# Performance work log

Measured on AMD Instinct MI355X. Metric: run time of the kernel, lower is better.

## Reference

```python
import jax, jax.numpy as jnp
import numpy as np

N = 100_000   # total vertices
E = 1_600_000 # total directed edges
B = 64        # graphs in batch
HID = 128
DM = 256
EPS = 1e-5


def _linear_init(k, fan_in, fan_out):
    lim = 1.0 / np.sqrt(fan_in)
    kw, kb = jax.random.split(k)
    W = jax.random.uniform(kw, (fan_in, fan_out), minval=-lim, maxval=lim, dtype=jnp.float32)
    b = jax.random.uniform(kb, (fan_out,), minval=-lim, maxval=lim, dtype=jnp.float32)
    return W, b


def setup_inputs() -> dict:
    key = jax.random.key(0)
    ks = jax.random.split(key, 8)
    W_in, b_in = _linear_init(ks[0], 3, HID)
    W1, b1 = _linear_init(ks[1], HID, HID)
    W2, b2 = _linear_init(ks[2], HID, HID)
    W3, b3 = _linear_init(ks[3], HID, HID)
    W_out, b_out = _linear_init(ks[4], HID, DM)
    vertices = jax.random.normal(ks[5], (N, 3), dtype=jnp.float32)
    edge_index = jax.random.randint(ks[6], (2, E), 0, N)
    batch = jnp.sort(jax.random.randint(ks[7], (N,), 0, B))
    gamma = jnp.ones((DM,), jnp.float32)
    beta = jnp.zeros((DM,), jnp.float32)
    return dict(vertices=vertices, edge_index=edge_index, batch=batch,
                W_in=W_in, b_in=b_in, W1=W1, b1=b1, W2=W2, b2=b2, W3=W3, b3=b3,
                W_out=W_out, b_out=b_out, gamma=gamma, beta=beta)


def _gcn_conv(x, W, b, src, dst):
    # PyG GCNConv: add self-loops, sym-normalize by deg^{-1/2}, aggregate at dst.
    h = x @ W  # [N, HID]
    deg = jnp.zeros((x.shape[0],), x.dtype).at[dst].add(1.0) + 1.0  # +1 self-loop
    dinv = jax.lax.rsqrt(deg)
    msg = h[src] * (dinv[src] * dinv[dst])[:, None]       # [E, HID] gather+scale
    agg = jnp.zeros_like(h).at[dst].add(msg)               # scatter-add
    agg = agg + h * (dinv * dinv)[:, None]                 # self-loop contribution
    return agg + b


def reference(vertices, edge_index, batch, W_in, b_in, W1, b1, W2, b2, W3, b3, W_out, b_out, gamma, beta):
    src, dst = edge_index[0], edge_index[1]
    x = vertices @ W_in + b_in
    for W, b in ((W1, b1), (W2, b2), (W3, b3)):
        x = jax.nn.relu(_gcn_conv(x, W, b, src, dst))
    # global_mean_pool over batch segments
    summ = jax.ops.segment_sum(x, batch, num_segments=B)
    cnt = jax.ops.segment_sum(jnp.ones((x.shape[0], 1), x.dtype), batch, num_segments=B)
    pooled = summ / jnp.maximum(cnt, 1.0)
    y = pooled @ W_out + b_out
    mu = jnp.mean(y, axis=-1, keepdims=True)
    var = jnp.var(y, axis=-1, keepdims=True)
    return (y - mu) * jax.lax.rsqrt(var + EPS) * gamma + beta
```

## Files before the change

kernel.cpp:

```cpp
#include <hip/hip_runtime.h>

constexpr int NV = 100000;
constexpr int NE = 1600000;
constexpr int NB = 64;
constexpr int HD = 128;
constexpr int DM = 256;
#define EPSLN 1e-5f

constexpr int DPB   = 512;
constexpr int NBUCK = (NV + DPB - 1) / DPB;
constexpr int EPB   = 4096;
constexpr int NEB   = (NE + EPB - 1) / EPB;

typedef short bf16x8 __attribute__((ext_vector_type(8)));
typedef float f32x4 __attribute__((ext_vector_type(4)));

__device__ inline unsigned short f2b(float f) {
    union { float f; unsigned u; } x; x.f = f;
    unsigned r = x.u + 0x7FFF + ((x.u >> 16) & 1);
    return (unsigned short)(r >> 16);
}
__device__ inline float b2f(unsigned short h) {
    union { unsigned u; float f; } x; x.u = (unsigned)h << 16;
    return x.f;
}

__global__ __launch_bounds__(256) void k_bhist(const int* __restrict__ ei,
                                               int* __restrict__ bcount) {
    __shared__ int h[NBUCK];
    int t = threadIdx.x;
    for (int i = t; i < NBUCK; i += 256) h[i] = 0;
    __syncthreads();
    int base = blockIdx.x * EPB;
    #pragma unroll
    for (int j = 0; j < EPB / 256; ++j) {
        int idx = base + j * 256 + t;
        if (idx < NE) atomicAdd(&h[ei[NE + idx] >> 9], 1);
    }
    __syncthreads();
    for (int i = t; i < NBUCK; i += 256) if (h[i]) atomicAdd(&bcount[i], h[i]);
}

__global__ void k_bscan(const int* __restrict__ bcount, int* __restrict__ bstart,
                        int* __restrict__ bcursor) {
    if (threadIdx.x == 0 && blockIdx.x == 0) {
        int run = 0;
        for (int i = 0; i < NBUCK; ++i) { bstart[i] = run; bcursor[i] = run; run += bcount[i]; }
        bstart[NBUCK] = run;
    }
}

__global__ __launch_bounds__(256) void k_bscatter(const int* __restrict__ ei,
                                                  int* __restrict__ bcursor,
                                                  int2* __restrict__ ebuf) {
    __shared__ int h[NBUCK];
    __shared__ int lbase[NBUCK];
    int t = threadIdx.x;
    for (int i = t; i < NBUCK; i += 256) h[i] = 0;
    __syncthreads();
    int base = blockIdx.x * EPB;
    int s[16], d[16], rk[16];
    #pragma unroll
    for (int j = 0; j < 16; ++j) {
        int idx = base + j * 256 + t;
        if (idx < NE) {
            s[j] = ei[idx];
            d[j] = ei[NE + idx];
            rk[j] = atomicAdd(&h[d[j] >> 9], 1);
        } else d[j] = -1;
    }
    __syncthreads();
    for (int i = t; i < NBUCK; i += 256) {
        int c = h[i];
        if (c) lbase[i] = atomicAdd(&bcursor[i], c);
    }
    __syncthreads();
    #pragma unroll
    for (int j = 0; j < 16; ++j)
        if (d[j] >= 0) ebuf[lbase[d[j] >> 9] + rk[j]] = make_int2(s[j], d[j]);
}

__global__ __launch_bounds__(256) void k_bcsr(const int2* __restrict__ ebuf,
                                              const int* __restrict__ bstart,
                                              int* __restrict__ degi,
                                              float* __restrict__ dinv,
                                              int* __restrict__ rowstart,
                                              int* __restrict__ csr) {
    __shared__ int h[DPB];
    __shared__ int sdata[256];
    int b = blockIdx.x, t = threadIdx.x, d0 = b * DPB;
    for (int i = t; i < DPB; i += 256) h[i] = 0;
    __syncthreads();
    int e0 = bstart[b], e1 = bstart[b + 1];
    for (int e = e0 + t; e < e1; e += 256) atomicAdd(&h[ebuf[e].y - d0], 1);
    __syncthreads();
    int a = h[2 * t], c = h[2 * t + 1];
    sdata[t] = a + c;
    __syncthreads();
    for (int off = 1; off < 256; off <<= 1) {
        int v = sdata[t];
        int add = (t >= off) ? sdata[t - off] : 0;
        __syncthreads();
        sdata[t] = v + add;
        __syncthreads();
    }
    int excl = (t == 0) ? 0 : sdata[t - 1];
    int base = bstart[b];
    int v0 = d0 + 2 * t, v1 = v0 + 1;
    if (v0 < NV) { rowstart[v0] = base + excl;     degi[v0] = a; dinv[v0] = rsqrtf((float)a + 1.0f); }
    if (v1 < NV) { rowstart[v1] = base + excl + a; degi[v1] = c; dinv[v1] = rsqrtf((float)c + 1.0f); }
    h[2 * t]     = base + excl;
    h[2 * t + 1] = base + excl + a;
    __syncthreads();
    for (int e = e0 + t; e < e1; e += 256) {
        int2 ed = ebuf[e];
        int slot = atomicAdd(&h[ed.y - d0], 1);
        csr[slot] = ed.x;
    }
}

__global__ void k_wc(const float* __restrict__ Win, const float* __restrict__ bin,
                     const float* __restrict__ W1, float* __restrict__ Wc,
                     float* __restrict__ bc) {
    int c = threadIdx.x;
    float w0 = 0.f, w1 = 0.f, w2 = 0.f, bv = 0.f;
    for (int k = 0; k < HD; ++k) {
        float w = W1[k * HD + c];
        w0 = fmaf(Win[k], w, w0);
        w1 = fmaf(Win[128 + k], w, w1);
        w2 = fmaf(Win[256 + k], w, w2);
        bv = fmaf(bin[k], w, bv);
    }
    Wc[c] = w0; Wc[128 + c] = w1; Wc[256 + c] = w2; bc[c] = bv;
}

__global__ void k_h1(const float* __restrict__ verts, const float* __restrict__ Wc,
                     const float* __restrict__ bc, unsigned short* __restrict__ Hb) {
    int idx = blockIdx.x * 256 + threadIdx.x;
    if (idx >= NV * HD) return;
    int v = idx >> 7, c = idx & 127;
    float a = verts[v * 3 + 0], b = verts[v * 3 + 1], d = verts[v * 3 + 2];
    Hb[idx] = f2b(bc[c] + a * Wc[c] + b * Wc[128 + c] + d * Wc[256 + c]);
}

__global__ void k_wt2(const float* __restrict__ W2, const float* __restrict__ W3,
                      unsigned short* __restrict__ Wt) {
    int idx = blockIdx.x * 256 + threadIdx.x;
    if (idx >= 2 * HD * HD) return;
    int l = idx >> 14, r = idx & 16383;
    const float* W = (l == 0) ? W2 : W3;
    int n = r >> 7, k = r & 127;
    Wt[idx - r + n * HD + k] = f2b(W[k * HD + n]);
}

__global__ __launch_bounds__(256) void k_gemm_mfma(const unsigned short* __restrict__ Xb,
                                                   const unsigned short* __restrict__ Wt,
                                                   unsigned short* __restrict__ Hb) {
    int wave = threadIdx.x >> 6;
    int lane = threadIdx.x & 63;
    int r = lane & 15;
    int g = lane >> 4;
    int row0 = blockIdx.x * 64 + wave * 16;
    int arow = row0 + r;
    bool valid = arow < NV;

    bf16x8 afrag[4];
    const unsigned short* xp = Xb + (size_t)arow * HD + g * 8;
    #pragma unroll
    for (int ks = 0; ks < 4; ++ks) {
        if (valid) afrag[ks] = *(const bf16x8*)(xp + ks * 32);
        else       afrag[ks] = bf16x8{0, 0, 0, 0, 0, 0, 0, 0};
    }

    #pragma unroll
    for (int nt = 0; nt < 8; ++nt) {
        f32x4 acc = {0.f, 0.f, 0.f, 0.f};
        const unsigned short* wp = Wt + (size_t)(nt * 16 + r) * HD + g * 8;
        #pragma unroll
        for (int ks = 0; ks < 4; ++ks) {
            bf16x8 bfrag = *(const bf16x8*)(wp + ks * 32);
            acc = __builtin_amdgcn_mfma_f32_16x16x32_bf16(afrag[ks], bfrag, acc, 0, 0, 0);
        }
        #pragma unroll
        for (int j = 0; j < 4; ++j) {
            int row = row0 + g * 4 + j;
            if (row < NV)
                Hb[(size_t)row * HD + nt * 16 + r] = f2b(acc[j]);
        }
    }
}

__global__ __launch_bounds__(256) void k_agg(const unsigned short* __restrict__ H,
                                             const float* __restrict__ dinv,
                                             const int* __restrict__ rowstart,
                                             const int* __restrict__ degi,
                                             const int* __restrict__ csr_src,
                                             const float* __restrict__ bias,
                                             unsigned short* __restrict__ Xo) {
    int gtid = blockIdx.x * 256 + threadIdx.x;
    int v = gtid >> 6;
    if (v >= NV) return;
    int lane = threadIdx.x & 63;
    int q = lane >> 4;
    int l4 = lane & 15;
    float di = dinv[v];
    int rs = rowstart[v], len = degi[v];
    float a[8];
    if (q == 0) {
        float sc = di * di;
        bf16x8 hv = *(const bf16x8*)(H + (size_t)v * HD + l4 * 8);
        #pragma unroll
        for (int jj = 0; jj < 8; ++jj) a[jj] = b2f((unsigned short)hv[jj]) * sc;
    } else {
        #pragma unroll
        for (int jj = 0; jj < 8; ++jj) a[jj] = 0.f;
    }
    int cnt = (len - q + 3) >> 2;
    int idx = rs + q;
    int j = 0;
    for (; j + 1 < cnt; j += 2) {
        int s0 = csr_src[idx], s1 = csr_src[idx + 4];
        idx += 8;
        float w0 = dinv[s0] * di, w1 = dinv[s1] * di;
        bf16x8 h0 = *(const bf16x8*)(H + (size_t)s0 * HD + l4 * 8);
        bf16x8 h1 = *(const bf16x8*)(H + (size_t)s1 * HD + l4 * 8);
        #pragma unroll
        for (int jj = 0; jj < 8; ++jj) {
            a[jj] = fmaf(b2f((unsigned short)h0[jj]), w0, a[jj]);
            a[jj] = fmaf(b2f((unsigned short)h1[jj]), w1, a[jj]);
        }
    }
    if (j < cnt) {
        int s0 = csr_src[idx];
        float w0 = dinv[s0] * di;
        bf16x8 h0 = *(const bf16x8*)(H + (size_t)s0 * HD + l4 * 8);
        #pragma unroll
        for (int jj = 0; jj < 8; ++jj)
            a[jj] = fmaf(b2f((unsigned short)h0[jj]), w0, a[jj]);
    }
    #pragma unroll
    for (int jj = 0; jj < 8; ++jj) {
        a[jj] += __shfl_xor(a[jj], 16);
        a[jj] += __shfl_xor(a[jj], 32);
    }
    if (q == 0) {
        bf16x8 ov;
        #pragma unroll
        for (int jj = 0; jj < 8; ++jj)
            ov[jj] = (short)f2b(fmaxf(a[jj] + bias[l4 * 8 + jj], 0.f));
        *(bf16x8*)(Xo + (size_t)v * HD + l4 * 8) = ov;
    }
}

__global__ __launch_bounds__(256) void k_pool(const unsigned short* __restrict__ X,
                                              const int* __restrict__ batch,
                                              float* __restrict__ pool,
                                              int* __restrict__ cnt) {
    constexpr int NCHUNK = 2048;
    constexpr int CHUNK = (NV + NCHUNK - 1) / NCHUNK;
    int c = threadIdx.x & 127;
    int r = threadIdx.x >> 7;
    int v0 = blockIdx.x * CHUNK;
    if (v0 >= NV) return;
    int vend = min(v0 + CHUNK, NV);
    int cur = -1;
    float sum = 0.f;
    for (int v = v0 + r; v < vend; v += 2) {
        int bb = batch[v];
        if (bb != cur) {
            if (cur >= 0) atomicAdd(&pool[cur * HD + c], sum);
            cur = bb; sum = 0.f;
        }
        sum += b2f(X[(size_t)v * HD + c]);
    }
    if (cur >= 0) atomicAdd(&pool[cur * HD + c], sum);
    if (threadIdx.x == 0) {
        int prev = batch[v0]; int c0 = 0;
        for (int v = v0; v < vend; ++v) {
            int bb = batch[v];
            if (bb != prev) { atomicAdd(&cnt[prev], c0); prev = bb; c0 = 0; }
            ++c0;
        }
        atomicAdd(&cnt[prev], c0);
    }
}

__global__ __launch_bounds__(256) void k_out(const float* __restrict__ pool,
                                             const int* __restrict__ cnt,
                                             const float* __restrict__ Wout,
                                             const float* __restrict__ bout,
                                             const float* __restrict__ gamma,
                                             const float* __restrict__ beta,
                                             float* __restrict__ out) {
    __shared__ float ps[HD];
    __shared__ float red[DM];
    int g = blockIdx.x, t = threadIdx.x;
    if (t < HD) {
        float cn = fmaxf((float)cnt[g], 1.0f);
        ps[t] = pool[g * HD + t] / cn;
    }
    __syncthreads();
    float acc = bout[t];
    #pragma unroll 8
    for (int k = 0; k < HD; ++k) acc = fmaf(ps[k], Wout[k * DM + t], acc);
    red[t] = acc; __syncthreads();
    for (int s2 = 128; s2 > 0; s2 >>= 1) {
        if (t < s2) red[t] += red[t + s2];
        __syncthreads();
    }
    float mu = red[0] * (1.0f / DM);
    __syncthreads();
    float d = acc - mu;
    red[t] = d * d; __syncthreads();
    for (int s2 = 128; s2 > 0; s2 >>= 1) {
        if (t < s2) red[t] += red[t + s2];
        __syncthreads();
    }
    float var = red[0] * (1.0f / DM);
    out[g * DM + t] = d * rsqrtf(var + EPSLN) * gamma[t] + beta[t];
}

extern "C" void kernel_launch(void* const* d_in, const int* in_sizes, int n_in,
                              void* d_out, int out_size, void* d_ws, size_t ws_size,
                              hipStream_t stream) {
    const float* verts = (const float*)d_in[0];
    const int*   ei    = (const int*)d_in[1];
    const int*   batch = (const int*)d_in[2];
    const float* Win   = (const float*)d_in[3];
    const float* bin   = (const float*)d_in[4];
    const float* W1    = (const float*)d_in[5];
    const float* b1    = (const float*)d_in[6];
    const float* W2    = (const float*)d_in[7];
    const float* b2    = (const float*)d_in[8];
    const float* W3    = (const float*)d_in[9];
    const float* b3    = (const float*)d_in[10];
    const float* Wout  = (const float*)d_in[11];
    const float* bout  = (const float*)d_in[12];
    const float* gamma = (const float*)d_in[13];
    const float* beta  = (const float*)d_in[14];
    float* out = (float*)d_out;

    char* wp = (char*)d_ws;
    auto alloc = [&](size_t bytes) -> char* {
        char* p = wp;
        wp += (bytes + 255) & ~(size_t)255;
        return p;
    };
    unsigned short* Xb  = (unsigned short*)alloc((size_t)NV * HD * 2);
    unsigned short* Hb  = (unsigned short*)alloc((size_t)NV * HD * 2);
    unsigned short* Wt  = (unsigned short*)alloc((size_t)2 * HD * HD * 2);
    float* Wc       = (float*)alloc((size_t)3 * HD * 4);
    float* bc       = (float*)alloc((size_t)HD * 4);
    int*   degi     = (int*)alloc((size_t)NV * 4);
    float* dinv     = (float*)alloc((size_t)NV * 4);
    int*   rowstart = (int*)alloc((size_t)NV * 4);
    int*   csr      = (int*)alloc((size_t)NE * 4);
    int2*  ebuf     = (int2*)alloc((size_t)NE * 8);
    int*   bcount   = (int*)alloc((size_t)NBUCK * 4);
    int*   bstart   = (int*)alloc((size_t)(NBUCK + 1) * 4);
    int*   bcursor  = (int*)alloc((size_t)NBUCK * 4);
    float* pool     = (float*)alloc((size_t)NB * HD * 4);
    int*   cnt      = (int*)alloc((size_t)NB * 4);

    hipMemsetAsync(bcount, 0, (size_t)NBUCK * 4, stream);
    hipMemsetAsync(pool,   0, (size_t)NB * HD * 4, stream);
    hipMemsetAsync(cnt,    0, (size_t)NB * 4, stream);

    k_bhist<<<NEB, 256, 0, stream>>>(ei, bcount);
    k_bscan<<<1, 64, 0, stream>>>(bcount, bstart, bcursor);
    k_bscatter<<<NEB, 256, 0, stream>>>(ei, bcursor, ebuf);
    k_bcsr<<<NBUCK, 256, 0, stream>>>(ebuf, bstart, degi, dinv, rowstart, csr);

    k_wc<<<1, 128, 0, stream>>>(Win, bin, W1, Wc, bc);
    k_wt2<<<(2 * HD * HD + 255) / 256, 256, 0, stream>>>(W2, W3, Wt);
    k_h1<<<((size_t)NV * HD + 255) / 256, 256, 0, stream>>>(verts, Wc, bc, Hb);

    k_agg<<<((size_t)NV * 64 + 255) / 256, 256, 0, stream>>>(Hb, dinv, rowstart, degi, csr, b1, Xb);
    const float* bl[2] = {b2, b3};
    for (int l = 0; l < 2; ++l) {
        k_gemm_mfma<<<(NV + 63) / 64, 256, 0, stream>>>(Xb, Wt + (size_t)l * HD * HD, Hb);
        k_agg<<<((size_t)NV * 64 + 255) / 256, 256, 0, stream>>>(Hb, dinv, rowstart, degi, csr, bl[l], Xb);
    }

    k_pool<<<2048, 256, 0, stream>>>(Xb, batch, pool, cnt);
    k_out<<<NB, 256, 0, stream>>>(pool, cnt, Wout, bout, gamma, beta, out);
}
```

Before: 398.6 us.

## Precompute per-edge normalization weights into CSR and pack edge buffer

The bucketed edge buffer now packs source and local destination into one int, which halves its size. CSR construction is split into two kernels, and the second stores (src, weight) pairs with dinv[src]*dinv[dst] computed once per edge. The aggregation kernel then skips the per-edge dinv gather on each of the three layers, and its inner loop is unrolled to four edges for more memory-level parallelism. In exchange the CSR entries double in size, the agg kernels read more bytes per edge, and there is one extra kernel launch. The packing assumes src << 9 fits in an int, which holds for 100k vertices.

```diff
diff --git a/kernel.cpp b/kernel.cpp
--- a/kernel.cpp
+++ b/kernel.cpp
@@ -52,7 +52,7 @@
 
 __global__ __launch_bounds__(256) void k_bscatter(const int* __restrict__ ei,
                                                   int* __restrict__ bcursor,
-                                                  int2* __restrict__ ebuf) {
+                                                  int* __restrict__ ebuf) {
     __shared__ int h[NBUCK];
     __shared__ int lbase[NBUCK];
     int t = threadIdx.x;
@@ -77,22 +77,21 @@
     __syncthreads();
     #pragma unroll
     for (int j = 0; j < 16; ++j)
-        if (d[j] >= 0) ebuf[lbase[d[j] >> 9] + rk[j]] = make_int2(s[j], d[j]);
-}
-
-__global__ __launch_bounds__(256) void k_bcsr(const int2* __restrict__ ebuf,
-                                              const int* __restrict__ bstart,
-                                              int* __restrict__ degi,
-                                              float* __restrict__ dinv,
-                                              int* __restrict__ rowstart,
-                                              int* __restrict__ csr) {
+        if (d[j] >= 0) ebuf[lbase[d[j] >> 9] + rk[j]] = (s[j] << 9) | (d[j] & 511);
+}
+
+__global__ __launch_bounds__(256) void k_bcsr_a(const int* __restrict__ ebuf,
+                                                const int* __restrict__ bstart,
+                                                int* __restrict__ degi,
+                                                float* __restrict__ dinv,
+                                                int* __restrict__ rowstart) {
     __shared__ int h[DPB];
     __shared__ int sdata[256];
     int b = blockIdx.x, t = threadIdx.x, d0 = b * DPB;
     for (int i = t; i < DPB; i += 256) h[i] = 0;
     __syncthreads();
     int e0 = bstart[b], e1 = bstart[b + 1];
-    for (int e = e0 + t; e < e1; e += 256) atomicAdd(&h[ebuf[e].y - d0], 1);
+    for (int e = e0 + t; e < e1; e += 256) atomicAdd(&h[ebuf[e] & 511], 1);
     __syncthreads();
     int a = h[2 * t], c = h[2 * t + 1];
     sdata[t] = a + c;
@@ -109,13 +108,30 @@
     int v0 = d0 + 2 * t, v1 = v0 + 1;
     if (v0 < NV) { rowstart[v0] = base + excl;     degi[v0] = a; dinv[v0] = rsqrtf((float)a + 1.0f); }
     if (v1 < NV) { rowstart[v1] = base + excl + a; degi[v1] = c; dinv[v1] = rsqrtf((float)c + 1.0f); }
-    h[2 * t]     = base + excl;
-    h[2 * t + 1] = base + excl + a;
-    __syncthreads();
+}
+
+__global__ __launch_bounds__(256) void k_bcsr_b(const int* __restrict__ ebuf,
+                                                const int* __restrict__ bstart,
+                                                const int* __restrict__ rowstart,
+                                                const float* __restrict__ dinv,
+                                                int2* __restrict__ csw) {
+    __shared__ int cur[DPB];
+    __shared__ float dlv[DPB];
+    int b = blockIdx.x, t = threadIdx.x, d0 = b * DPB;
+    for (int i = t; i < DPB; i += 256) {
+        int v = d0 + i;
+        cur[i] = (v < NV) ? rowstart[v] : 0;
+        dlv[i] = (v < NV) ? dinv[v] : 0.f;
+    }
+    __syncthreads();
+    int e0 = bstart[b], e1 = bstart[b + 1];
     for (int e = e0 + t; e < e1; e += 256) {
-        int2 ed = ebuf[e];
-        int slot = atomicAdd(&h[ed.y - d0], 1);
-        csr[slot] = ed.x;
+        int p = ebuf[e];
+        int s = p >> 9;
+        int dl = p & 511;
+        int slot = atomicAdd(&cur[dl], 1);
+        float w = dinv[s] * dlv[dl];
+        csw[slot] = make_int2(s, __float_as_int(w));
     }
 }
 
@@ -194,7 +210,7 @@
                                              const float* __restrict__ dinv,
                                              const int* __restrict__ rowstart,
                                              const int* __restrict__ degi,
-                                             const int* __restrict__ csr_src,
+                                             const int2* __restrict__ csw,
                                              const float* __restrict__ bias,
                                              unsigned short* __restrict__ Xo) {
     int gtid = blockIdx.x * 256 + threadIdx.x;
@@ -203,10 +219,10 @@
     int lane = threadIdx.x & 63;
     int q = lane >> 4;
     int l4 = lane & 15;
-    float di = dinv[v];
     int rs = rowstart[v], len = degi[v];
     float a[8];
     if (q == 0) {
+        float di = dinv[v];
         float sc = di * di;
         bf16x8 hv = *(const bf16x8*)(H + (size_t)v * HD + l4 * 8);
         #pragma unroll
@@ -218,22 +234,28 @@
     int cnt = (len - q + 3) >> 2;
     int idx = rs + q;
     int j = 0;
-    for (; j + 1 < cnt; j += 2) {
-        int s0 = csr_src[idx], s1 = csr_src[idx + 4];
-        idx += 8;
-        float w0 = dinv[s0] * di, w1 = dinv[s1] * di;
-        bf16x8 h0 = *(const bf16x8*)(H + (size_t)s0 * HD + l4 * 8);
-        bf16x8 h1 = *(const bf16x8*)(H + (size_t)s1 * HD + l4 * 8);
+    for (; j + 3 < cnt; j += 4) {
+        int2 e0 = csw[idx], e1 = csw[idx + 4], e2 = csw[idx + 8], e3 = csw[idx + 12];
+        idx += 16;
+        bf16x8 h0 = *(const bf16x8*)(H + (size_t)e0.x * HD + l4 * 8);
+        bf16x8 h1 = *(const bf16x8*)(H + (size_t)e1.x * HD + l4 * 8);
+        bf16x8 h2 = *(const bf16x8*)(H + (size_t)e2.x * HD + l4 * 8);
+        bf16x8 h3 = *(const bf16x8*)(H + (size_t)e3.x * HD + l4 * 8);
+        float w0 = __int_as_float(e0.y), w1 = __int_as_float(e1.y);
+        float w2 = __int_as_float(e2.y), w3 = __int_as_float(e3.y);
         #pragma unroll
         for (int jj = 0; jj < 8; ++jj) {
             a[jj] = fmaf(b2f((unsigned short)h0[jj]), w0, a[jj]);
             a[jj] = fmaf(b2f((unsigned short)h1[jj]), w1, a[jj]);
+            a[jj] = fmaf(b2f((unsigned short)h2[jj]), w2, a[jj]);
+            a[jj] = fmaf(b2f((unsigned short)h3[jj]), w3, a[jj]);
         }
     }
-    if (j < cnt) {
-        int s0 = csr_src[idx];
-        float w0 = dinv[s0] * di;
-        bf16x8 h0 = *(const bf16x8*)(H + (size_t)s0 * HD + l4 * 8);
+    for (; j < cnt; ++j) {
+        int2 e0 = csw[idx];
+        idx += 4;
+        float w0 = __int_as_float(e0.y);
+        bf16x8 h0 = *(const bf16x8*)(H + (size_t)e0.x * HD + l4 * 8);
         #pragma unroll
         for (int jj = 0; jj < 8; ++jj)
             a[jj] = fmaf(b2f((unsigned short)h0[jj]), w0, a[jj]);
@@ -354,8 +376,8 @@
     int*   degi     = (int*)alloc((size_t)NV * 4);
     float* dinv     = (float*)alloc((size_t)NV * 4);
     int*   rowstart = (int*)alloc((size_t)NV * 4);
-    int*   csr      = (int*)alloc((size_t)NE * 4);
-    int2*  ebuf     = (int2*)alloc((size_t)NE * 8);
+    int2*  csw      = (int2*)alloc((size_t)NE * 8);
+    int*   ebuf     = (int*)alloc((size_t)NE * 4);
     int*   bcount   = (int*)alloc((size_t)NBUCK * 4);
     int*   bstart   = (int*)alloc((size_t)(NBUCK + 1) * 4);
     int*   bcursor  = (int*)alloc((size_t)NBUCK * 4);
@@ -369,17 +391,18 @@
     k_bhist<<<NEB, 256, 0, stream>>>(ei, bcount);
     k_bscan<<<1, 64, 0, stream>>>(bcount, bstart, bcursor);
     k_bscatter<<<NEB, 256, 0, stream>>>(ei, bcursor, ebuf);
-    k_bcsr<<<NBUCK, 256, 0, stream>>>(ebuf, bstart, degi, dinv, rowstart, csr);
+    k_bcsr_a<<<NBUCK, 256, 0, stream>>>(ebuf, bstart, degi, dinv, rowstart);
+    k_bcsr_b<<<NBUCK, 256, 0, stream>>>(ebuf, bstart, rowstart, dinv, csw);
 
     k_wc<<<1, 128, 0, stream>>>(Win, bin, W1, Wc, bc);
     k_wt2<<<(2 * HD * HD + 255) / 256, 256, 0, stream>>>(W2, W3, Wt);
     k_h1<<<((size_t)NV * HD + 255) / 256, 256, 0, stream>>>(verts, Wc, bc, Hb);
 
-    k_agg<<<((size_t)NV * 64 + 255) / 256, 256, 0, stream>>>(Hb, dinv, rowstart, degi, csr, b1, Xb);
+    k_agg<<<((size_t)NV * 64 + 255) / 256, 256, 0, stream>>>(Hb, dinv, rowstart, degi, csw, b1, Xb);
     const float* bl[2] = {b2, b3};
     for (int l = 0; l < 2; ++l) {
         k_gemm_mfma<<<(NV + 63) / 64, 256, 0, stream>>>(Xb, Wt + (size_t)l * HD * HD, Hb);
-        k_agg<<<((size_t)NV * 64 + 255) / 256, 256, 0, stream>>>(Hb, dinv, rowstart, degi, csr, bl[l], Xb);
+        k_agg<<<((size_t)NV * 64 + 255) / 256, 256, 0, stream>>>(Hb, dinv, rowstart, degi, csw, bl[l], Xb);
     }
 
     k_pool<<<2048, 256, 0, stream>>>(Xb, batch, pool, cnt);
```

Result: no change. 406.3 us (+1.9%).

## Fuse aggregation with next-layer MFMA GEMM, pack edge buffer, merge weight-combine into h1

Applied to the files above, without the earlier changes.

Each of the first two GCN aggregations now writes its relu output for 16 rows per wave into LDS and immediately runs the next layer's bf16 MFMA GEMM. This removes a full-size intermediate write and read plus two kernel launches. Edges in the bucket buffer are packed into one int (source<<9 | local dst), which halves that buffer's traffic. The Win·W1 weight combine is folded into k_h1, which now uses a grid-stride loop. The risk is that the fused kernel runs one wave per 16 vertices serially, with four quarter-waves splitting each vertex's edges, which may lower memory parallelism compared with the old one-wave-per-vertex aggregation.

```diff
diff --git a/kernel.cpp b/kernel.cpp
--- a/kernel.cpp
+++ b/kernel.cpp
@@ -52,7 +52,7 @@
 
 __global__ __launch_bounds__(256) void k_bscatter(const int* __restrict__ ei,
                                                   int* __restrict__ bcursor,
-                                                  int2* __restrict__ ebuf) {
+                                                  int* __restrict__ ebuf) {
     __shared__ int h[NBUCK];
     __shared__ int lbase[NBUCK];
     int t = threadIdx.x;
@@ -77,10 +77,10 @@
     __syncthreads();
     #pragma unroll
     for (int j = 0; j < 16; ++j)
-        if (d[j] >= 0) ebuf[lbase[d[j] >> 9] + rk[j]] = make_int2(s[j], d[j]);
-}
-
-__global__ __launch_bounds__(256) void k_bcsr(const int2* __restrict__ ebuf,
+        if (d[j] >= 0) ebuf[lbase[d[j] >> 9] + rk[j]] = (s[j] << 9) | (d[j] & 511);
+}
+
+__global__ __launch_bounds__(256) void k_bcsr(const int* __restrict__ ebuf,
                                               const int* __restrict__ bstart,
                                               int* __restrict__ degi,
                                               float* __restrict__ dinv,
@@ -92,7 +92,7 @@
     for (int i = t; i < DPB; i += 256) h[i] = 0;
     __syncthreads();
     int e0 = bstart[b], e1 = bstart[b + 1];
-    for (int e = e0 + t; e < e1; e += 256) atomicAdd(&h[ebuf[e].y - d0], 1);
+    for (int e = e0 + t; e < e1; e += 256) atomicAdd(&h[ebuf[e] & 511], 1);
     __syncthreads();
     int a = h[2 * t], c = h[2 * t + 1];
     sdata[t] = a + c;
@@ -113,34 +113,37 @@
     h[2 * t + 1] = base + excl + a;
     __syncthreads();
     for (int e = e0 + t; e < e1; e += 256) {
-        int2 ed = ebuf[e];
-        int slot = atomicAdd(&h[ed.y - d0], 1);
-        csr[slot] = ed.x;
-    }
-}
-
-__global__ void k_wc(const float* __restrict__ Win, const float* __restrict__ bin,
-                     const float* __restrict__ W1, float* __restrict__ Wc,
-                     float* __restrict__ bc) {
-    int c = threadIdx.x;
-    float w0 = 0.f, w1 = 0.f, w2 = 0.f, bv = 0.f;
-    for (int k = 0; k < HD; ++k) {
-        float w = W1[k * HD + c];
-        w0 = fmaf(Win[k], w, w0);
-        w1 = fmaf(Win[128 + k], w, w1);
-        w2 = fmaf(Win[256 + k], w, w2);
-        bv = fmaf(bin[k], w, bv);
-    }
-    Wc[c] = w0; Wc[128 + c] = w1; Wc[256 + c] = w2; bc[c] = bv;
-}
-
-__global__ void k_h1(const float* __restrict__ verts, const float* __restrict__ Wc,
-                     const float* __restrict__ bc, unsigned short* __restrict__ Hb) {
-    int idx = blockIdx.x * 256 + threadIdx.x;
-    if (idx >= NV * HD) return;
-    int v = idx >> 7, c = idx & 127;
-    float a = verts[v * 3 + 0], b = verts[v * 3 + 1], d = verts[v * 3 + 2];
-    Hb[idx] = f2b(bc[c] + a * Wc[c] + b * Wc[128 + c] + d * Wc[256 + c]);
+        int p = ebuf[e];
+        int slot = atomicAdd(&h[p & 511], 1);
+        csr[slot] = p >> 9;
+    }
+}
+
+__global__ __launch_bounds__(256) void k_h1(const float* __restrict__ verts,
+                                            const float* __restrict__ Win,
+                                            const float* __restrict__ bin,
+                                            const float* __restrict__ W1,
+                                            unsigned short* __restrict__ Hb) {
+    __shared__ float Wc[3 * HD];
+    __shared__ float bc[HD];
+    int t = threadIdx.x;
+    if (t < HD) {
+        float w0 = 0.f, w1 = 0.f, w2 = 0.f, bv = 0.f;
+        for (int k = 0; k < HD; ++k) {
+            float w = W1[k * HD + t];
+            w0 = fmaf(Win[k], w, w0);
+            w1 = fmaf(Win[128 + k], w, w1);
+            w2 = fmaf(Win[256 + k], w, w2);
+            bv = fmaf(bin[k], w, bv);
+        }
+        Wc[t] = w0; Wc[128 + t] = w1; Wc[256 + t] = w2; bc[t] = bv;
+    }
+    __syncthreads();
+    for (int idx = blockIdx.x * 256 + t; idx < NV * HD; idx += gridDim.x * 256) {
+        int v = idx >> 7, c = idx & 127;
+        float a = verts[v * 3 + 0], b = verts[v * 3 + 1], d = verts[v * 3 + 2];
+        Hb[idx] = f2b(bc[c] + a * Wc[c] + b * Wc[128 + c] + d * Wc[256 + c]);
+    }
 }
 
 __global__ void k_wt2(const float* __restrict__ W2, const float* __restrict__ W3,
@@ -153,29 +156,83 @@
     Wt[idx - r + n * HD + k] = f2b(W[k * HD + n]);
 }
 
-__global__ __launch_bounds__(256) void k_gemm_mfma(const unsigned short* __restrict__ Xb,
-                                                   const unsigned short* __restrict__ Wt,
-                                                   unsigned short* __restrict__ Hb) {
+__global__ __launch_bounds__(256) void k_aggf(const unsigned short* __restrict__ H,
+                                              const float* __restrict__ dinv,
+                                              const int* __restrict__ rowstart,
+                                              const int* __restrict__ degi,
+                                              const int* __restrict__ csr_src,
+                                              const float* __restrict__ bias,
+                                              const unsigned short* __restrict__ Wt,
+                                              unsigned short* __restrict__ Hout) {
+    __shared__ __align__(16) unsigned short xt[4][16][136];
     int wave = threadIdx.x >> 6;
     int lane = threadIdx.x & 63;
-    int r = lane & 15;
-    int g = lane >> 4;
-    int row0 = blockIdx.x * 64 + wave * 16;
-    int arow = row0 + r;
-    bool valid = arow < NV;
+    int q = lane >> 4;
+    int l4 = lane & 15;
+    int v0 = blockIdx.x * 64 + wave * 16;
+    if (v0 >= NV) return;
+
+    for (int r = 0; r < 16; ++r) {
+        int v = v0 + r;
+        if (v >= NV) break;
+        float di = dinv[v];
+        int rs = rowstart[v], len = degi[v];
+        float a[8];
+        if (q == 0) {
+            float sc = di * di;
+            bf16x8 hv = *(const bf16x8*)(H + (size_t)v * HD + l4 * 8);
+            #pragma unroll
+            for (int jj = 0; jj < 8; ++jj) a[jj] = b2f((unsigned short)hv[jj]) * sc;
+        } else {
+            #pragma unroll
+            for (int jj = 0; jj < 8; ++jj) a[jj] = 0.f;
+        }
+        int cnt = (len - q + 3) >> 2;
+        int idx = rs + q;
+        int j = 0;
+        for (; j + 1 < cnt; j += 2) {
+            int s0 = csr_src[idx], s1 = csr_src[idx + 4];
+            idx += 8;
+            float w0 = dinv[s0] * di, w1 = dinv[s1] * di;
+            bf16x8 h0 = *(const bf16x8*)(H + (size_t)s0 * HD + l4 * 8);
+            bf16x8 h1 = *(const bf16x8*)(H + (size_t)s1 * HD + l4 * 8);
+            #pragma unroll
+            for (int jj = 0; jj < 8; ++jj) {
+                a[jj] = fmaf(b2f((unsigned short)h0[jj]), w0, a[jj]);
+                a[jj] = fmaf(b2f((unsigned short)h1[jj]), w1, a[jj]);
+            }
+        }
+        if (j < cnt) {
+            int s0 = csr_src[idx];
+            float w0 = dinv[s0] * di;
+            bf16x8 h0 = *(const bf16x8*)(H + (size_t)s0 * HD + l4 * 8);
+            #pragma unroll
+            for (int jj = 0; jj < 8; ++jj)
+                a[jj] = fmaf(b2f((unsigned short)h0[jj]), w0, a[jj]);
+        }
+        #pragma unroll
+        for (int jj = 0; jj < 8; ++jj) {
+            a[jj] += __shfl_xor(a[jj], 16);
+            a[jj] += __shfl_xor(a[jj], 32);
+        }
+        if (q == 0) {
+            bf16x8 ov;
+            #pragma unroll
+            for (int jj = 0; jj < 8; ++jj)
+                ov[jj] = (short)f2b(fmaxf(a[jj] + bias[l4 * 8 + jj], 0.f));
+            *(bf16x8*)&xt[wave][r][l4 * 8] = ov;
+        }
+    }
 
     bf16x8 afrag[4];
-    const unsigned short* xp = Xb + (size_t)arow * HD + g * 8;
-    #pragma unroll
-    for (int ks = 0; ks < 4; ++ks) {
-        if (valid) afrag[ks] = *(const bf16x8*)(xp + ks * 32);
-        else       afrag[ks] = bf16x8{0, 0, 0, 0, 0, 0, 0, 0};
-    }
+    #pragma unroll
+    for (int ks = 0; ks < 4; ++ks)
+        afrag[ks] = *(const bf16x8*)&xt[wave][l4][q * 8 + ks * 32];
 
     #pragma unroll
     for (int nt = 0; nt < 8; ++nt) {
         f32x4 acc = {0.f, 0.f, 0.f, 0.f};
-        const unsigned short* wp = Wt + (size_t)(nt * 16 + r) * HD + g * 8;
+        const unsigned short* wp = Wt + (size_t)(nt * 16 + l4) * HD + q * 8;
         #pragma unroll
         for (int ks = 0; ks < 4; ++ks) {
             bf16x8 bfrag = *(const bf16x8*)(wp + ks * 32);
@@ -183,9 +240,9 @@
         }
         #pragma unroll
         for (int j = 0; j < 4; ++j) {
-            int row = row0 + g * 4 + j;
+            int row = v0 + q * 4 + j;
             if (row < NV)
-                Hb[(size_t)row * HD + nt * 16 + r] = f2b(acc[j]);
+                Hout[(size_t)row * HD + nt * 16 + l4] = f2b(acc[j]);
         }
     }
 }
@@ -346,16 +403,14 @@
         wp += (bytes + 255) & ~(size_t)255;
         return p;
     };
-    unsigned short* Xb  = (unsigned short*)alloc((size_t)NV * HD * 2);
-    unsigned short* Hb  = (unsigned short*)alloc((size_t)NV * HD * 2);
-    unsigned short* Wt  = (unsigned short*)alloc((size_t)2 * HD * HD * 2);
-    float* Wc       = (float*)alloc((size_t)3 * HD * 4);
-    float* bc       = (float*)alloc((size_t)HD * 4);
+    unsigned short* bufA = (unsigned short*)alloc((size_t)NV * HD * 2);
+    unsigned short* bufB = (unsigned short*)alloc((size_t)NV * HD * 2);
+    unsigned short* Wt   = (unsigned short*)alloc((size_t)2 * HD * HD * 2);
     int*   degi     = (int*)alloc((size_t)NV * 4);
     float* dinv     = (float*)alloc((size_t)NV * 4);
     int*   rowstart = (int*)alloc((size_t)NV * 4);
     int*   csr      = (int*)alloc((size_t)NE * 4);
-    int2*  ebuf     = (int2*)alloc((size_t)NE * 8);
+    int*   ebuf     = (int*)alloc((size_t)NE * 4);
     int*   bcount   = (int*)alloc((size_t)NBUCK * 4);
     int*   bstart   = (int*)alloc((size_t)(NBUCK + 1) * 4);
     int*   bcursor  = (int*)alloc((size_t)NBUCK * 4);
@@ -371,17 +426,13 @@
     k_bscatter<<<NEB, 256, 0, stream>>>(ei, bcursor, ebuf);
     k_bcsr<<<NBUCK, 256, 0, stream>>>(ebuf, bstart, degi, dinv, rowstart, csr);
 
-    k_wc<<<1, 128, 0, stream>>>(Win, bin, W1, Wc, bc);
     k_wt2<<<(2 * HD * HD + 255) / 256, 256, 0, stream>>>(W2, W3, Wt);
-    k_h1<<<((size_t)NV * HD + 255) / 256, 256, 0, stream>>>(verts, Wc, bc, Hb);
-
-    k_agg<<<((size_t)NV * 64 + 255) / 256, 256, 0, stream>>>(Hb, dinv, rowstart, degi, csr, b1, Xb);
-    const float* bl[2] = {b2, b3};
-    for (int l = 0; l < 2; ++l) {
-        k_gemm_mfma<<<(NV + 63) / 64, 256, 0, stream>>>(Xb, Wt + (size_t)l * HD * HD, Hb);
-        k_agg<<<((size_t)NV * 64 + 255) / 256, 256, 0, stream>>>(Hb, dinv, rowstart, degi, csr, bl[l], Xb);
-    }
-
-    k_pool<<<2048, 256, 0, stream>>>(Xb, batch, pool, cnt);
+    k_h1<<<1024, 256, 0, stream>>>(verts, Win, bin, W1, bufA);
+
+    k_aggf<<<(NV + 63) / 64, 256, 0, stream>>>(bufA, dinv, rowstart, degi, csr, b1, Wt, bufB);
+    k_aggf<<<(NV + 63) / 64, 256, 0, stream>>>(bufB, dinv, rowstart, degi, csr, b2, Wt + (size_t)HD * HD, bufA);
+    k_agg<<<((size_t)NV * 64 + 255) / 256, 256, 0, stream>>>(bufA, dinv, rowstart, degi, csr, b3, bufB);
+
+    k_pool<<<2048, 256, 0, stream>>>(bufB, batch, pool, cnt);
     k_out<<<NB, 256, 0, stream>>>(pool, cnt, Wout, bout, gamma, beta, out);
 }
```

New measurement: 370.2 us. -7.1%, faster.

## Split aggregation into column halves, pack edge buffer, fuse weight combine into h1

Applied to the files above, without the earlier changes.

The aggregation kernel now handles 64 of the 128 feature columns per launch and is run twice per layer. Each wave covers 8 edges at a time with 8 lanes per row segment, so the gathered working set per pass is half as large and should cache better. The bucketed edge buffer packs src and dst-low-bits into one int, which halves that intermediate's traffic. The Win·W1 combine is folded into a grid-stride k_h1 through shared memory. In exchange, the CSR indices and dinv are read twice per layer, and the packing assumes src fits in 23 bits.

```diff
diff --git a/kernel.cpp b/kernel.cpp
--- a/kernel.cpp
+++ b/kernel.cpp
@@ -52,7 +52,7 @@
 
 __global__ __launch_bounds__(256) void k_bscatter(const int* __restrict__ ei,
                                                   int* __restrict__ bcursor,
-                                                  int2* __restrict__ ebuf) {
+                                                  int* __restrict__ ebuf) {
     __shared__ int h[NBUCK];
     __shared__ int lbase[NBUCK];
     int t = threadIdx.x;
@@ -77,10 +77,10 @@
     __syncthreads();
     #pragma unroll
     for (int j = 0; j < 16; ++j)
-        if (d[j] >= 0) ebuf[lbase[d[j] >> 9] + rk[j]] = make_int2(s[j], d[j]);
-}
-
-__global__ __launch_bounds__(256) void k_bcsr(const int2* __restrict__ ebuf,
+        if (d[j] >= 0) ebuf[lbase[d[j] >> 9] + rk[j]] = (s[j] << 9) | (d[j] & 511);
+}
+
+__global__ __launch_bounds__(256) void k_bcsr(const int* __restrict__ ebuf,
                                               const int* __restrict__ bstart,
                                               int* __restrict__ degi,
                                               float* __restrict__ dinv,
@@ -92,7 +92,7 @@
     for (int i = t; i < DPB; i += 256) h[i] = 0;
     __syncthreads();
     int e0 = bstart[b], e1 = bstart[b + 1];
-    for (int e = e0 + t; e < e1; e += 256) atomicAdd(&h[ebuf[e].y - d0], 1);
+    for (int e = e0 + t; e < e1; e += 256) atomicAdd(&h[ebuf[e] & 511], 1);
     __syncthreads();
     int a = h[2 * t], c = h[2 * t + 1];
     sdata[t] = a + c;
@@ -113,34 +113,37 @@
     h[2 * t + 1] = base + excl + a;
     __syncthreads();
     for (int e = e0 + t; e < e1; e += 256) {
-        int2 ed = ebuf[e];
-        int slot = atomicAdd(&h[ed.y - d0], 1);
-        csr[slot] = ed.x;
-    }
-}
-
-__global__ void k_wc(const float* __restrict__ Win, const float* __restrict__ bin,
-                     const float* __restrict__ W1, float* __restrict__ Wc,
-                     float* __restrict__ bc) {
-    int c = threadIdx.x;
-    float w0 = 0.f, w1 = 0.f, w2 = 0.f, bv = 0.f;
-    for (int k = 0; k < HD; ++k) {
-        float w = W1[k * HD + c];
-        w0 = fmaf(Win[k], w, w0);
-        w1 = fmaf(Win[128 + k], w, w1);
-        w2 = fmaf(Win[256 + k], w, w2);
-        bv = fmaf(bin[k], w, bv);
-    }
-    Wc[c] = w0; Wc[128 + c] = w1; Wc[256 + c] = w2; bc[c] = bv;
-}
-
-__global__ void k_h1(const float* __restrict__ verts, const float* __restrict__ Wc,
-                     const float* __restrict__ bc, unsigned short* __restrict__ Hb) {
-    int idx = blockIdx.x * 256 + threadIdx.x;
-    if (idx >= NV * HD) return;
-    int v = idx >> 7, c = idx & 127;
-    float a = verts[v * 3 + 0], b = verts[v * 3 + 1], d = verts[v * 3 + 2];
-    Hb[idx] = f2b(bc[c] + a * Wc[c] + b * Wc[128 + c] + d * Wc[256 + c]);
+        int p = ebuf[e];
+        int slot = atomicAdd(&h[p & 511], 1);
+        csr[slot] = p >> 9;
+    }
+}
+
+__global__ __launch_bounds__(256) void k_h1(const float* __restrict__ verts,
+                                            const float* __restrict__ Win,
+                                            const float* __restrict__ bin,
+                                            const float* __restrict__ W1,
+                                            unsigned short* __restrict__ Hb) {
+    __shared__ float Wc[3 * HD];
+    __shared__ float bc[HD];
+    int t = threadIdx.x;
+    if (t < HD) {
+        float w0 = 0.f, w1 = 0.f, w2 = 0.f, bv = 0.f;
+        for (int k = 0; k < HD; ++k) {
+            float w = W1[k * HD + t];
+            w0 = fmaf(Win[k], w, w0);
+            w1 = fmaf(Win[128 + k], w, w1);
+            w2 = fmaf(Win[256 + k], w, w2);
+            bv = fmaf(bin[k], w, bv);
+        }
+        Wc[t] = w0; Wc[128 + t] = w1; Wc[256 + t] = w2; bc[t] = bv;
+    }
+    __syncthreads();
+    for (int idx = blockIdx.x * 256 + t; idx < NV * HD; idx += gridDim.x * 256) {
+        int v = idx >> 7, c = idx & 127;
+        float a = verts[v * 3 + 0], b = verts[v * 3 + 1], d = verts[v * 3 + 2];
+        Hb[idx] = f2b(bc[c] + a * Wc[c] + b * Wc[128 + c] + d * Wc[256 + c]);
+    }
 }
 
 __global__ void k_wt2(const float* __restrict__ W2, const float* __restrict__ W3,
@@ -196,34 +199,36 @@
                                              const int* __restrict__ degi,
                                              const int* __restrict__ csr_src,
                                              const float* __restrict__ bias,
-                                             unsigned short* __restrict__ Xo) {
+                                             unsigned short* __restrict__ Xo,
+                                             int colbase) {
     int gtid = blockIdx.x * 256 + threadIdx.x;
     int v = gtid >> 6;
     if (v >= NV) return;
     int lane = threadIdx.x & 63;
-    int q = lane >> 4;
-    int l4 = lane & 15;
+    int g = lane >> 3;
+    int l3 = lane & 7;
+    const unsigned short* Hc = H + colbase;
     float di = dinv[v];
     int rs = rowstart[v], len = degi[v];
     float a[8];
-    if (q == 0) {
+    if (g == 0) {
         float sc = di * di;
-        bf16x8 hv = *(const bf16x8*)(H + (size_t)v * HD + l4 * 8);
+        bf16x8 hv = *(const bf16x8*)(Hc + (size_t)v * HD + l3 * 8);
         #pragma unroll
         for (int jj = 0; jj < 8; ++jj) a[jj] = b2f((unsigned short)hv[jj]) * sc;
     } else {
         #pragma unroll
         for (int jj = 0; jj < 8; ++jj) a[jj] = 0.f;
     }
-    int cnt = (len - q + 3) >> 2;
-    int idx = rs + q;
+    int cnt = (len - g + 7) >> 3;
+    int idx = rs + g;
     int j = 0;
     for (; j + 1 < cnt; j += 2) {
-        int s0 = csr_src[idx], s1 = csr_src[idx + 4];
-        idx += 8;
+        int s0 = csr_src[idx], s1 = csr_src[idx + 8];
+        idx += 16;
         float w0 = dinv[s0] * di, w1 = dinv[s1] * di;
-        bf16x8 h0 = *(const bf16x8*)(H + (size_t)s0 * HD + l4 * 8);
-        bf16x8 h1 = *(const bf16x8*)(H + (size_t)s1 * HD + l4 * 8);
+        bf16x8 h0 = *(const bf16x8*)(Hc + (size_t)s0 * HD + l3 * 8);
+        bf16x8 h1 = *(const bf16x8*)(Hc + (size_t)s1 * HD + l3 * 8);
         #pragma unroll
         for (int jj = 0; jj < 8; ++jj) {
             a[jj] = fmaf(b2f((unsigned short)h0[jj]), w0, a[jj]);
@@ -233,22 +238,23 @@
     if (j < cnt) {
         int s0 = csr_src[idx];
         float w0 = dinv[s0] * di;
-        bf16x8 h0 = *(const bf16x8*)(H + (size_t)s0 * HD + l4 * 8);
+        bf16x8 h0 = *(const bf16x8*)(Hc + (size_t)s0 * HD + l3 * 8);
         #pragma unroll
         for (int jj = 0; jj < 8; ++jj)
             a[jj] = fmaf(b2f((unsigned short)h0[jj]), w0, a[jj]);
     }
     #pragma unroll
     for (int jj = 0; jj < 8; ++jj) {
+        a[jj] += __shfl_xor(a[jj], 8);
         a[jj] += __shfl_xor(a[jj], 16);
         a[jj] += __shfl_xor(a[jj], 32);
     }
-    if (q == 0) {
+    if (g == 0) {
         bf16x8 ov;
         #pragma unroll
         for (int jj = 0; jj < 8; ++jj)
-            ov[jj] = (short)f2b(fmaxf(a[jj] + bias[l4 * 8 + jj], 0.f));
-        *(bf16x8*)(Xo + (size_t)v * HD + l4 * 8) = ov;
+            ov[jj] = (short)f2b(fmaxf(a[jj] + bias[colbase + l3 * 8 + jj], 0.f));
+        *(bf16x8*)(Xo + (size_t)v * HD + colbase + l3 * 8) = ov;
     }
 }
 
@@ -346,16 +352,14 @@
         wp += (bytes + 255) & ~(size_t)255;
         return p;
     };
-    unsigned short* Xb  = (unsigned short*)alloc((size_t)NV * HD * 2);
-    unsigned short* Hb  = (unsigned short*)alloc((size_t)NV * HD * 2);
-    unsigned short* Wt  = (unsigned short*)alloc((size_t)2 * HD * HD * 2);
-    float* Wc       = (float*)alloc((size_t)3 * HD * 4);
-    float* bc       = (float*)alloc((size_t)HD * 4);
+    unsigned short* bufA = (unsigned short*)alloc((size_t)NV * HD * 2);
+    unsigned short* bufB = (unsigned short*)alloc((size_t)NV * HD * 2);
+    unsigned short* Wt   = (unsigned short*)alloc((size_t)2 * HD * HD * 2);
     int*   degi     = (int*)alloc((size_t)NV * 4);
     float* dinv     = (float*)alloc((size_t)NV * 4);
     int*   rowstart = (int*)alloc((size_t)NV * 4);
     int*   csr      = (int*)alloc((size_t)NE * 4);
-    int2*  ebuf     = (int2*)alloc((size_t)NE * 8);
+    int*   ebuf     = (int*)alloc((size_t)NE * 4);
     int*   bcount   = (int*)alloc((size_t)NBUCK * 4);
     int*   bstart   = (int*)alloc((size_t)(NBUCK + 1) * 4);
     int*   bcursor  = (int*)alloc((size_t)NBUCK * 4);
@@ -371,17 +375,19 @@
     k_bscatter<<<NEB, 256, 0, stream>>>(ei, bcursor, ebuf);
     k_bcsr<<<NBUCK, 256, 0, stream>>>(ebuf, bstart, degi, dinv, rowstart, csr);
 
-    k_wc<<<1, 128, 0, stream>>>(Win, bin, W1, Wc, bc);
     k_wt2<<<(2 * HD * HD + 255) / 256, 256, 0, stream>>>(W2, W3, Wt);
-    k_h1<<<((size_t)NV * HD + 255) / 256, 256, 0, stream>>>(verts, Wc, bc, Hb);
-
-    k_agg<<<((size_t)NV * 64 + 255) / 256, 256, 0, stream>>>(Hb, dinv, rowstart, degi, csr, b1, Xb);
-    const float* bl[2] = {b2, b3};
-    for (int l = 0; l < 2; ++l) {
-        k_gemm_mfma<<<(NV + 63) / 64, 256, 0, stream>>>(Xb, Wt + (size_t)l * HD * HD, Hb);
-        k_agg<<<((size_t)NV * 64 + 255) / 256, 256, 0, stream>>>(Hb, dinv, rowstart, degi, csr, bl[l], Xb);
-    }
-
-    k_pool<<<2048, 256, 0, stream>>>(Xb, batch, pool, cnt);
+    k_h1<<<1024, 256, 0, stream>>>(verts, Win, bin, W1, bufA);
+
+    int aggrid = (int)(((size_t)NV * 64 + 255) / 256);
+    k_agg<<<aggrid, 256, 0, stream>>>(bufA, dinv, rowstart, degi, csr, b1, bufB, 0);
+    k_agg<<<aggrid, 256, 0, stream>>>(bufA, dinv, rowstart, degi, csr, b1, bufB, 64);
+    k_gemm_mfma<<<(NV + 63) / 64, 256, 0, stream>>>(bufB, Wt, bufA);
+    k_agg<<<aggrid, 256, 0, stream>>>(bufA, dinv, rowstart, degi, csr, b2, bufB, 0);
+    k_agg<<<aggrid, 256, 0, stream>>>(bufA, dinv, rowstart, degi, csr, b2, bufB, 64);
+    k_gemm_mfma<<<(NV + 63) / 64, 256, 0, stream>>>(bufB, Wt + (size_t)HD * HD, bufA);
+    k_agg<<<aggrid, 256, 0, stream>>>(bufA, dinv, rowstart, degi, csr, b3, bufB, 0);
+    k_agg<<<aggrid, 256, 0, stream>>>(bufA, dinv, rowstart, degi, csr, b3, bufB, 64);
+
+    k_pool<<<2048, 256, 0, stream>>>(bufB, batch, pool, cnt);
     k_out<<<NB, 256, 0, stream>>>(pool, cnt, Wout, bout, gamma, beta, out);
 }
```

Result: slower. 477.3 us (+19.7%).
